# Kernel tuning notes

Measured on AMD Instinct MI355X. Metric: run time of the kernel, lower is better.

## Reference

```python
import jax, jax.numpy as jnp
import numpy as np

NEG_INF = -1.0e9  # matches torch masked_fill constant in topk_mean_pooling


def setup_inputs() -> dict:
    key = jax.random.key(0)
    k1, k2 = jax.random.split(key)
    h = jax.random.normal(k1, (8, 4096, 512), dtype=jnp.float32)
    patch_ids = jnp.sort(jax.random.randint(k2, (8, 4096), 0, 1024), axis=-1)
    return {"h": h, "patch_ids": patch_ids, "max_num_patches": 1024, "k": 4}


def reference(h, patch_ids, max_num_patches, k):
    """topk_mean_pooling / pooling_downsample('topk:k') from ByteLatentEncoder.

    h:          [bs, seq_len, dim] float
    patch_ids:  [bs, seq_len] int, values in [0, max_num_patches)
    returns:    [bs, max_num_patches, dim]
    """
    bs, seq_len, dim = h.shape
    P = max_num_patches
    b_idx = jnp.arange(bs)[:, None]  # [bs, 1], broadcasts against patch_ids

    # tokens per patch (one_hot.sum(1) in torch)
    counts = jnp.zeros((bs, P), h.dtype).at[b_idx, patch_ids].add(jnp.ones((), h.dtype))

    h_work = h
    collected = []
    for _ in range(k):  # k is a small fixed constant (from 'topk:N')
        # scatter_reduce(amax, include_self=False): untargeted patches stay 0
        cm = jnp.full((bs, P, dim), -jnp.inf, h.dtype).at[b_idx, patch_ids].max(h_work)
        cm = jnp.where(jnp.isinf(cm), jnp.zeros((), h.dtype), cm)
        collected.append(cm)
        # gather current max back to token positions and knock out all ties
        gathered = cm[b_idx, patch_ids]  # [bs, seq_len, dim]
        h_work = jnp.where(h_work == gathered, jnp.asarray(NEG_INF, h.dtype), h_work)

    topk_vals = jnp.stack(collected, axis=2)  # [bs, P, k, dim]
    # only the first count_p iterations are valid for patch p
    valid = (jnp.arange(k)[None, None, :] < counts[:, :, None]).astype(h.dtype)  # [bs, P, k]
    sum_valid = (topk_vals * valid[..., None]).sum(axis=2)  # [bs, P, dim]
    num_valid = jnp.clip(valid.sum(axis=2), 1.0)[..., None]
    return sum_valid / num_valid
```

## Files before the change

### kernel.cpp

```cpp
#include <hip/hip_runtime.h>
#include <math.h>

#define BS   8
#define SEQ  4096
#define DIM  512
#define NP   1024
#define KTOP 4
#define NEGINF_C (-1.0e9f)

typedef float f32x4 __attribute__((ext_vector_type(4)));

__device__ __forceinline__ void ins5(float v, float& m0, float& m1, float& m2,
                                     float& m3, float& m4) {
    float a;
    a = fmaxf(m0, v); v = fminf(m0, v); m0 = a;
    a = fmaxf(m1, v); v = fminf(m1, v); m1 = a;
    a = fmaxf(m2, v); v = fminf(m2, v); m2 = a;
    a = fmaxf(m3, v); v = fminf(m3, v); m3 = a;
    m4 = fmaxf(m4, v);
}

#define INS5V(v)                                   \
    do {                                           \
        ins5((v).x, a0, a1, a2, a3, a4);           \
        ins5((v).y, b0, b1, b2, b3, b4);           \
        ins5((v).z, c0, c1, c2, c3, c4);           \
        ins5((v).w, d0, d1, d2, d3, d4);           \
    } while (0)

__device__ __forceinline__ float dedup_avg(float s0, float s1, float s2, float s3,
                                           float s4, int n, float inv_n) {
    const bool e1 = (s1 == s0) & (s1 != -INFINITY);
    const bool e2 = (s2 == s1) & (s2 != -INFINITY);
    const bool e3 = (s3 == s2) & (s3 != -INFINITY);
    const float o1 = e1 ? s2 : s1;
    const float o2 = (e1 | e2) ? s3 : s2;
    const float o3 = (e1 | e2 | e3) ? s4 : s3;
    float acc = (s0 == -INFINITY) ? NEGINF_C : s0;
    if (n > 1) acc += (o1 == -INFINITY) ? NEGINF_C : o1;
    if (n > 2) acc += (o2 == -INFINITY) ? NEGINF_C : o2;
    if (n > 3) acc += (o3 == -INFINITY) ? NEGINF_C : o3;
    return acc * inv_n;
}

__device__ __forceinline__ float small_avg(float v0, float v1, float v2, float v3,
                                           int cnt, float inv_n) {
    const float c1 = (v1 == v0) ? NEGINF_C : v1;
    const float c2 = ((v2 == v0) | (v2 == v1)) ? NEGINF_C : v2;
    const float c3 = ((v3 == v0) | (v3 == v1) | (v3 == v2)) ? NEGINF_C : v3;
    float acc = v0;
    if (cnt > 1) acc += c1;
    if (cnt > 2) acc += c2;
    if (cnt > 3) acc += c3;
    return acc * inv_n;
}

__global__ __launch_bounds__(128) void topk_pool_kernel(const float* __restrict__ h,
                                                        const int* __restrict__ pid,
                                                        float* __restrict__ out) {
    const int bp   = blockIdx.x;
    const int b    = bp >> 10;
    const int p    = bp & (NP - 1);
    const int tid  = threadIdx.x;
    const int lane = tid & 63;
    const int* ids = pid + b * SEQ;

    const int probe1 = lane << 6;
    const unsigned long long m1 = __ballot(ids[probe1] < p);
    const int c1 = __popcll(m1);
    const int base = (c1 == 0) ? 0 : ((c1 - 1) << 6) + 1;

    const int idx2  = base + lane;
    const int idx2c = (idx2 < SEQ) ? idx2 : (SEQ - 1);
    const bool lt2  = (idx2 < SEQ) && (ids[idx2c] < p);
    const int start = base + __popcll(__ballot(lt2));

    const int i3  = start + lane;
    const int i3c = (i3 < SEQ) ? i3 : (SEQ - 1);
    const bool eq = (i3 < SEQ) && (ids[i3c] == p);
    int cnt = __popcll(__ballot(eq));
    if (cnt == 64) {
        int off64 = 64;
        while (true) {
            const int i  = start + off64 + lane;
            const int ic = (i < SEQ) ? i : (SEQ - 1);
            const bool e = (i < SEQ) && (ids[ic] == p);
            const int cc = __popcll(__ballot(e));
            cnt += cc;
            if (cc < 64) break;
            off64 += 64;
        }
    }

    f32x4* outv = (f32x4*)(out + ((size_t)b * NP + p) * DIM);

    if (cnt == 0) {
        __builtin_nontemporal_store((f32x4){0.f, 0.f, 0.f, 0.f}, &outv[tid]);
        return;
    }

    const f32x4* hr = (const f32x4*)(h + (size_t)b * SEQ * DIM)
                      + (size_t)start * (DIM / 4) + tid;
    const int n = (cnt < KTOP) ? cnt : KTOP;
    const float inv_n = 1.0f / (float)n;

    if (cnt <= KTOP) {
        const int o1 = ((1 < cnt) ? 1 : (cnt - 1)) * (DIM / 4);
        const int o2 = ((2 < cnt) ? 2 : (cnt - 1)) * (DIM / 4);
        const int o3 = ((3 < cnt) ? 3 : (cnt - 1)) * (DIM / 4);
        const f32x4 v0 = hr[0];
        const f32x4 v1 = hr[o1];
        const f32x4 v2 = hr[o2];
        const f32x4 v3 = hr[o3];
        f32x4 r;
        r.x = small_avg(v0.x, v1.x, v2.x, v3.x, cnt, inv_n);
        r.y = small_avg(v0.y, v1.y, v2.y, v3.y, cnt, inv_n);
        r.z = small_avg(v0.z, v1.z, v2.z, v3.z, cnt, inv_n);
        r.w = small_avg(v0.w, v1.w, v2.w, v3.w, cnt, inv_n);
        __builtin_nontemporal_store(r, &outv[tid]);
        return;
    }

    float a0 = -INFINITY, a1 = -INFINITY, a2 = -INFINITY, a3 = -INFINITY, a4 = -INFINITY;
    float b0 = -INFINITY, b1 = -INFINITY, b2 = -INFINITY, b3 = -INFINITY, b4 = -INFINITY;
    float c0 = -INFINITY, c1f = -INFINITY, c2 = -INFINITY, c3 = -INFINITY, c4 = -INFINITY;
    float d0 = -INFINITY, d1 = -INFINITY, d2 = -INFINITY, d3 = -INFINITY, d4 = -INFINITY;

    int rem = cnt;
    int off = 0;
    for (; rem >= 4; rem -= 4, off += 4 * (DIM / 4)) {
        const f32x4 w0 = hr[off];
        const f32x4 w1 = hr[off + 1 * (DIM / 4)];
        const f32x4 w2 = hr[off + 2 * (DIM / 4)];
        const f32x4 w3 = hr[off + 3 * (DIM / 4)];
        ins5(w0.x, a0, a1, a2, a3, a4); ins5(w0.y, b0, b1, b2, b3, b4);
        ins5(w0.z, c0, c1f, c2, c3, c4); ins5(w0.w, d0, d1, d2, d3, d4);
        ins5(w1.x, a0, a1, a2, a3, a4); ins5(w1.y, b0, b1, b2, b3, b4);
        ins5(w1.z, c0, c1f, c2, c3, c4); ins5(w1.w, d0, d1, d2, d3, d4);
        ins5(w2.x, a0, a1, a2, a3, a4); ins5(w2.y, b0, b1, b2, b3, b4);
        ins5(w2.z, c0, c1f, c2, c3, c4); ins5(w2.w, d0, d1, d2, d3, d4);
        ins5(w3.x, a0, a1, a2, a3, a4); ins5(w3.y, b0, b1, b2, b3, b4);
        ins5(w3.z, c0, c1f, c2, c3, c4); ins5(w3.w, d0, d1, d2, d3, d4);
    }
    for (; rem > 0; --rem, off += (DIM / 4)) {
        const f32x4 w = hr[off];
        ins5(w.x, a0, a1, a2, a3, a4); ins5(w.y, b0, b1, b2, b3, b4);
        ins5(w.z, c0, c1f, c2, c3, c4); ins5(w.w, d0, d1, d2, d3, d4);
    }

    f32x4 r;
    r.x = dedup_avg(a0, a1, a2, a3, a4, n, inv_n);
    r.y = dedup_avg(b0, b1, b2, b3, b4, n, inv_n);
    r.z = dedup_avg(c0, c1f, c2, c3, c4, n, inv_n);
    r.w = dedup_avg(d0, d1, d2, d3, d4, n, inv_n);
    __builtin_nontemporal_store(r, &outv[tid]);
}

extern "C" void kernel_launch(void* const* d_in, const int* in_sizes, int n_in,
                              void* d_out, int out_size, void* d_ws, size_t ws_size,
                              hipStream_t stream) {
    const float* h   = (const float*)d_in[0];
    const int*   pid = (const int*)d_in[1];
    float*       out = (float*)d_out;
    (void)d_ws; (void)ws_size;

    topk_pool_kernel<<<dim3(BS * NP), dim3(128), 0, stream>>>(h, pid, out);
}
```

Baseline: 21.14 us.

## Precompute patch start offsets in a separate boundaries kernel

Adds a small pre-pass kernel that writes each patch's start index into workspace by detecting changes in the sorted patch ids. The main pooling kernel then reads start and end directly instead of running a three-stage ballot search over patch_ids for every block. This removes the dependent global loads and wave reductions before the h loads can start, at the cost of an extra kernel launch and a dependency through workspace memory.

```diff
diff --git a/kernel.cpp b/kernel.cpp
--- a/kernel.cpp
+++ b/kernel.cpp
@@ -10,6 +10,22 @@
 
 typedef float f32x4 __attribute__((ext_vector_type(4)));
 
+__global__ __launch_bounds__(256) void boundaries_kernel(const int* __restrict__ pid,
+                                                         int* __restrict__ starts) {
+    const int gt = blockIdx.x * 256 + threadIdx.x;
+    const int b  = gt / SEQ;
+    const int t  = gt - b * SEQ;
+    const int* ids = pid + b * SEQ;
+    int* st = starts + b * (NP + 1);
+
+    const int cur  = ids[t];
+    const int prev = (t > 0) ? ids[t - 1] : -1;
+    for (int p = prev + 1; p <= cur; ++p) st[p] = t;
+    if (t == SEQ - 1) {
+        for (int p = cur + 1; p <= NP; ++p) st[p] = SEQ;
+    }
+}
+
 __device__ __forceinline__ void ins5(float v, float& m0, float& m1, float& m2,
                                      float& m3, float& m4) {
     float a;
@@ -19,14 +35,6 @@
     a = fmaxf(m3, v); v = fminf(m3, v); m3 = a;
     m4 = fmaxf(m4, v);
 }
-
-#define INS5V(v)                                   \
-    do {                                           \
-        ins5((v).x, a0, a1, a2, a3, a4);           \
-        ins5((v).y, b0, b1, b2, b3, b4);           \
-        ins5((v).z, c0, c1, c2, c3, c4);           \
-        ins5((v).w, d0, d1, d2, d3, d4);           \
-    } while (0)
 
 __device__ __forceinline__ float dedup_avg(float s0, float s1, float s2, float s3,
                                            float s4, int n, float inv_n) {
@@ -56,41 +64,17 @@
 }
 
 __global__ __launch_bounds__(128) void topk_pool_kernel(const float* __restrict__ h,
-                                                        const int* __restrict__ pid,
+                                                        const int* __restrict__ starts,
                                                         float* __restrict__ out) {
     const int bp   = blockIdx.x;
     const int b    = bp >> 10;
     const int p    = bp & (NP - 1);
     const int tid  = threadIdx.x;
-    const int lane = tid & 63;
-    const int* ids = pid + b * SEQ;
 
-    const int probe1 = lane << 6;
-    const unsigned long long m1 = __ballot(ids[probe1] < p);
-    const int c1 = __popcll(m1);
-    const int base = (c1 == 0) ? 0 : ((c1 - 1) << 6) + 1;
-
-    const int idx2  = base + lane;
-    const int idx2c = (idx2 < SEQ) ? idx2 : (SEQ - 1);
-    const bool lt2  = (idx2 < SEQ) && (ids[idx2c] < p);
-    const int start = base + __popcll(__ballot(lt2));
-
-    const int i3  = start + lane;
-    const int i3c = (i3 < SEQ) ? i3 : (SEQ - 1);
-    const bool eq = (i3 < SEQ) && (ids[i3c] == p);
-    int cnt = __popcll(__ballot(eq));
-    if (cnt == 64) {
-        int off64 = 64;
-        while (true) {
-            const int i  = start + off64 + lane;
-            const int ic = (i < SEQ) ? i : (SEQ - 1);
-            const bool e = (i < SEQ) && (ids[ic] == p);
-            const int cc = __popcll(__ballot(e));
-            cnt += cc;
-            if (cc < 64) break;
-            off64 += 64;
-        }
-    }
+    const int* st   = starts + b * (NP + 1);
+    const int start = st[p];
+    const int end   = st[p + 1];
+    const int cnt   = end - start;
 
     f32x4* outv = (f32x4*)(out + ((size_t)b * NP + p) * DIM);
 
@@ -162,7 +146,8 @@
     const float* h   = (const float*)d_in[0];
     const int*   pid = (const int*)d_in[1];
     float*       out = (float*)d_out;
-    (void)d_ws; (void)ws_size;
+    int*         starts = (int*)d_ws;
 
-    topk_pool_kernel<<<dim3(BS * NP), dim3(128), 0, stream>>>(h, pid, out);
+    boundaries_kernel<<<dim3((BS * SEQ) / 256), dim3(256), 0, stream>>>(pid, starts);
+    topk_pool_kernel<<<dim3(BS * NP), dim3(128), 0, stream>>>(h, starts, out);
 }
```

After: 24.49 us. +15.9%, slower.
